# Kernel optimization log

Hardware: AMD Instinct MI355X
Metric: run time of the kernel (lower is better)

## Reference

```python
import jax, jax.numpy as jnp
from jax import lax
import numpy as np

B, C, H, W = 8, 4, 512, 512
SIGMA, W0 = 5.0, 10.0
_DBIG = 1e6  # sentinel 1D distance (larger than any image diagonal)


def setup_inputs() -> dict:
    key = jax.random.key(0)
    k1, k2 = jax.random.split(key)
    pred = jax.random.normal(k1, (B, C, H, W), jnp.float32)
    labels = jax.random.randint(k2, (B, H, W), 0, C)
    target = jax.nn.one_hot(labels, C, axis=1, dtype=jnp.float32)  # (B,C,H,W) one-hot
    return {"pred": pred, "target": target}


def _edt_sq(mask):
    """Exact squared Euclidean distance transform to True pixels of a (H,W) bool mask.
    Equivalent to scipy.ndimage.distance_transform_edt(1 - mask)**2.
    Pass 1: exact 1D distance along axis 1 via forward/backward cummax of feature indices.
    Pass 2: min-plus envelope along axis 0: D2[i,j] = min_k g[k,j]^2 + (i-k)^2."""
    Hh, Ww = mask.shape
    col = jnp.arange(Ww, dtype=jnp.float32)
    # nearest feature index to the left / right within each row
    left = lax.cummax(jnp.where(mask, col, -_DBIG), axis=1)
    dl = col[None, :] - left
    rneg = lax.cummax(jnp.where(mask, -col, -_DBIG), axis=1, reverse=True)
    dr = -rneg - col[None, :]
    g = jnp.minimum(jnp.minimum(dl, dr), _DBIG)  # (H,W) 1D distance
    g2 = g * g
    rows = jnp.arange(Hh, dtype=jnp.float32)

    def step(D2, xs):
        g2k, k = xs  # row k's 1D squared distances
        cand = g2k[None, :] + (rows - k)[:, None] ** 2
        return jnp.minimum(D2, cand), None

    D2, _ = lax.scan(step, jnp.full((Hh, Ww), _DBIG * _DBIG, jnp.float32), (g2, rows))
    return D2


def _border_weights(target, sigma, w0):
    """U-Net border weight map: w = 1 + w0*exp(-(d1+d2)^2 / (2 sigma^2))."""
    label_map = jnp.argmax(target, axis=1)  # (B,H,W)
    Cn = target.shape[1]
    masks = label_map[:, None, :, :] == jnp.arange(Cn)[None, :, None, None]  # (B,C,H,W)
    # a class contributes a distance map only if it has both fg and bg pixels
    valid = masks.any(axis=(2, 3)) & (~masks).any(axis=(2, 3))  # (B,C)
    D2 = jax.vmap(jax.vmap(_edt_sq))(masks)  # (B,C,H,W)
    dist = jnp.where(valid[:, :, None, None], jnp.sqrt(D2), _DBIG)
    ds = jnp.sort(dist, axis=1)  # invalid classes sort to the end (sentinel)
    d1, d2 = ds[:, 0], ds[:, 1]
    # if fewer than 2 valid classes, d2 (and possibly d1) is the sentinel -> exp underflows to 0 -> w == 1,
    # matching the torch code's early-continue (weights stay 1).
    return 1.0 + w0 * jnp.exp(-((d1 + d2) ** 2) / (2.0 * sigma * sigma))


def reference(pred, target):
    logp = jax.nn.log_softmax(pred, axis=1)
    target_idx = jnp.argmax(target, axis=1)  # (B,H,W)
    per_pixel = -jnp.take_along_axis(logp, target_idx[:, None], axis=1)[:, 0]  # CE, reduction='none'
    w = lax.stop_gradient(_border_weights(target, SIGMA, W0))  # weights built from detached target
    weighted = jnp.mean(per_pixel * w)
    base = jnp.mean(-(target * logp).sum(axis=1))  # soft cross-entropy base loss
    return base + weighted
```

## Files before the change

### kernel.cpp

```cpp
#include <hip/hip_runtime.h>
#include <stdint.h>

#define HH 512
#define WW 512
#define CC 4
#define BB 8
#define NPIX (BB * HH * WW)
#define SLAB 8
#define NBLK (BB * HH / SLAB)

__device__ __forceinline__ float row_min_sq(uint32_t v) {
    float c0 = (float)(v & 255u);
    float c1 = (float)((v >> 8) & 255u);
    float c2 = (float)((v >> 16) & 255u);
    float c3 = (float)(v >> 24);
    return fminf(fminf(c0 * c0, c1 * c1), fminf(c2 * c2, c3 * c3));
}

__device__ __forceinline__ uint32_t own_mask(uint32_t v) {
    uint32_t z = (~((v & 0x7F7F7F7Fu) + 0x7F7F7F7Fu)) & ~v & 0x80808080u;
    return (z >> 7) * 255u;
}

__device__ __forceinline__ void scan_row(const float* __restrict__ trow,
                                         int lane, uint32_t* __restrict__ ldsrow) {
    const int j0 = lane << 3;

    int L[8];
    float tm[8];
    #pragma unroll
    for (int c = 0; c < CC; ++c) {
        const float4* p = reinterpret_cast<const float4*>(trow + (size_t)c * (HH * WW) + j0);
        float4 a0 = p[0], a1 = p[1];
        float tv[8] = {a0.x, a0.y, a0.z, a0.w, a1.x, a1.y, a1.z, a1.w};
        #pragma unroll
        for (int jj = 0; jj < 8; ++jj) {
            if (c == 0) { tm[jj] = tv[jj]; L[jj] = 0; }
            else if (tv[jj] > tm[jj]) { tm[jj] = tv[jj]; L[jj] = c; }
        }
    }

    uint32_t gp[8] = {0, 0, 0, 0, 0, 0, 0, 0};
    #pragma unroll
    for (int c = 0; c < CC; ++c) {
        int run = -1000000;
        int lastL[8];
        #pragma unroll
        for (int jj = 0; jj < 8; ++jj) { if (L[jj] == c) run = j0 + jj; lastL[jj] = run; }
        int incl = run;
        #pragma unroll
        for (int d = 1; d < 64; d <<= 1) {
            int up = __shfl_up(incl, (unsigned)d, 64);
            if (lane >= d) incl = max(incl, up);
        }
        int excl = __shfl_up(incl, 1u, 64);
        if (lane == 0) excl = -1000000;

        int nrun = 1000000;
        int nxtL[8];
        #pragma unroll
        for (int jj = 7; jj >= 0; --jj) { if (L[jj] == c) nrun = j0 + jj; nxtL[jj] = nrun; }
        int rincl = nrun;
        #pragma unroll
        for (int d = 1; d < 64; d <<= 1) {
            int dn = __shfl_down(rincl, (unsigned)d, 64);
            if (lane < 64 - d) rincl = min(rincl, dn);
        }
        int rexcl = __shfl_down(rincl, 1u, 64);
        if (lane == 63) rexcl = 1000000;

        #pragma unroll
        for (int jj = 0; jj < 8; ++jj) {
            int last = max(lastL[jj], excl);
            int nxt  = min(nxtL[jj], rexcl);
            int gg = min(min((j0 + jj) - last, nxt - (j0 + jj)), 255);
            gp[jj] |= ((uint32_t)gg) << (c * 8);
        }
    }
    uint4* o = reinterpret_cast<uint4*>(ldsrow + j0);
    o[0] = make_uint4(gp[0], gp[1], gp[2], gp[3]);
    o[1] = make_uint4(gp[4], gp[5], gp[6], gp[7]);
}

__global__ __launch_bounds__(512) void k_fused(const float* __restrict__ pred,
                                               const float* __restrict__ target,
                                               float* __restrict__ partial) {
    __shared__ uint32_t gl[12][WW];
    __shared__ float red[8];
    __shared__ int sflag;

    const int bid0 = blockIdx.x;
    const int bid = ((bid0 & 7) << 6) | (bid0 >> 3);
    const int b  = bid >> 6;
    const int i0 = (bid & 63) << 3;
    const int tid = threadIdx.x, wid = tid >> 6, lane = tid & 63;
    const float* tbase = target + (size_t)b * CC * (HH * WW);

    {
        int r = i0 - 2 + wid;
        if (r >= 0 && r < HH) scan_row(tbase + (size_t)r * WW, lane, gl[wid]);
        if (wid < 4) {
            int r2 = i0 + 6 + wid;
            if (r2 < HH) scan_row(tbase + (size_t)r2 * WW, lane, gl[8 + wid]);
        }
    }
    if (tid == 0) sflag = 0;
    __syncthreads();

    const int grp = tid >> 8;
    const int j   = (tid & 255) << 1;
    float    bs[4][2];
    uint32_t om[4][2];
    #pragma unroll
    for (int q = 0; q < 4; ++q) {
        const int s  = (grp << 2) + q;
        const int la = s + 2;
        uint2 gown = *reinterpret_cast<const uint2*>(&gl[la][j]);
        uint32_t o0 = own_mask(gown.x), o1 = own_mask(gown.y);
        float b0 = row_min_sq(gown.x | o0);
        float b1 = row_min_sq(gown.y | o1);
        #pragma unroll
        for (int dk = 1; dk <= 2; ++dk) {
            const float dk2 = (float)(dk * dk);
            if (i0 + s - dk >= 0) {
                uint2 v = *reinterpret_cast<const uint2*>(&gl[la - dk][j]);
                b0 = fminf(b0, row_min_sq(v.x | o0) + dk2);
                b1 = fminf(b1, row_min_sq(v.y | o1) + dk2);
            }
            if (i0 + s + dk < HH) {
                uint2 v = *reinterpret_cast<const uint2*>(&gl[la + dk][j]);
                b0 = fminf(b0, row_min_sq(v.x | o0) + dk2);
                b1 = fminf(b1, row_min_sq(v.y | o1) + dk2);
            }
        }
        bs[q][0] = b0; bs[q][1] = b1; om[q][0] = o0; om[q][1] = o1;
    }

    {
        float mx = 0.f;
        #pragma unroll
        for (int q = 0; q < 4; ++q) mx = fmaxf(mx, fmaxf(bs[q][0], bs[q][1]));
        if (__any(mx > 9.0f)) { if (lane == 0) sflag = 1; }
    }
    __syncthreads();

    if (sflag) {
        for (int dk = 3; dk < HH; ++dk) {
            { int rr = i0 + wid - dk;
              if (rr >= 0 && rr < HH) scan_row(tbase + (size_t)rr * WW, lane, gl[wid]); }
            __syncthreads();
            const float dk2 = (float)(dk * dk);
            #pragma unroll
            for (int q = 0; q < 4; ++q) {
                const int s = (grp << 2) + q;
                if (i0 + s - dk >= 0) {
                    uint2 v = *reinterpret_cast<const uint2*>(&gl[s][j]);
                    bs[q][0] = fminf(bs[q][0], row_min_sq(v.x | om[q][0]) + dk2);
                    bs[q][1] = fminf(bs[q][1], row_min_sq(v.y | om[q][1]) + dk2);
                }
            }
            __syncthreads();
            { int rr = i0 + wid + dk;
              if (rr < HH) scan_row(tbase + (size_t)rr * WW, lane, gl[wid]); }
            __syncthreads();
            #pragma unroll
            for (int q = 0; q < 4; ++q) {
                const int s = (grp << 2) + q;
                if (i0 + s + dk < HH) {
                    uint2 v = *reinterpret_cast<const uint2*>(&gl[s][j]);
                    bs[q][0] = fminf(bs[q][0], row_min_sq(v.x | om[q][0]) + dk2);
                    bs[q][1] = fminf(bs[q][1], row_min_sq(v.y | om[q][1]) + dk2);
                }
            }
            __syncthreads();
            if (tid == 0) sflag = 0;
            __syncthreads();
            float nthr = (float)((dk + 1) * (dk + 1));
            float mx = 0.f;
            #pragma unroll
            for (int q = 0; q < 4; ++q) mx = fmaxf(mx, fmaxf(bs[q][0], bs[q][1]));
            if (__any(mx > nthr)) { if (lane == 0) sflag = 1; }
            __syncthreads();
            if (!sflag) break;
            if (i0 + SLAB - 1 - dk < 0 && i0 + dk >= HH) break;
        }
    }

    const float* pb = pred + (((size_t)b * CC) * HH + (size_t)i0) * WW + j;
    float vacc = 0.f;
    #pragma unroll
    for (int q = 0; q < 4; ++q) {
        const int s = (grp << 2) + q;
        const float* pr = pb + (size_t)s * WW;
        float a0[CC], a1[CC];
        #pragma unroll
        for (int c = 0; c < CC; ++c) {
            float2 t = *reinterpret_cast<const float2*>(pr + (size_t)c * (HH * WW));
            a0[c] = t.x; a1[c] = t.y;
        }
        const int L0 = __builtin_ctz(om[q][0]) >> 3;
        const int L1 = __builtin_ctz(om[q][1]) >> 3;
        {
            float m = fmaxf(fmaxf(a0[0], a0[1]), fmaxf(a0[2], a0[3]));
            float ssum = __expf(a0[0] - m) + __expf(a0[1] - m) +
                         __expf(a0[2] - m) + __expf(a0[3] - m);
            float xs = (L0 == 0) ? a0[0] : (L0 == 1) ? a0[1] : (L0 == 2) ? a0[2] : a0[3];
            float pp = (m + __logf(ssum)) - xs;
            vacc += pp * fmaf(10.0f, __expf(-0.02f * bs[q][0]), 2.0f);
        }
        {
            float m = fmaxf(fmaxf(a1[0], a1[1]), fmaxf(a1[2], a1[3]));
            float ssum = __expf(a1[0] - m) + __expf(a1[1] - m) +
                         __expf(a1[2] - m) + __expf(a1[3] - m);
            float xs = (L1 == 0) ? a1[0] : (L1 == 1) ? a1[1] : (L1 == 2) ? a1[2] : a1[3];
            float pp = (m + __logf(ssum)) - xs;
            vacc += pp * fmaf(10.0f, __expf(-0.02f * bs[q][1]), 2.0f);
        }
    }

    #pragma unroll
    for (int off = 32; off > 0; off >>= 1) vacc += __shfl_down(vacc, (unsigned)off, 64);
    if (lane == 0) red[wid] = vacc;
    __syncthreads();
    if (tid == 0) {
        float bsum = ((red[0] + red[1]) + (red[2] + red[3]))
                   + ((red[4] + red[5]) + (red[6] + red[7]));
        partial[blockIdx.x] = bsum;
    }
}

__global__ __launch_bounds__(256) void k_red(const float* __restrict__ partial,
                                             float* __restrict__ out) {
    __shared__ double sd[256];
    double a = (double)partial[threadIdx.x] + (double)partial[threadIdx.x + 256];
    sd[threadIdx.x] = a;
    __syncthreads();
    #pragma unroll
    for (int s = 128; s > 0; s >>= 1) {
        if (threadIdx.x < s) sd[threadIdx.x] += sd[threadIdx.x + s];
        __syncthreads();
    }
    if (threadIdx.x == 0) out[0] = (float)(sd[0] * (1.0 / (double)NPIX));
}

extern "C" void kernel_launch(void* const* d_in, const int* in_sizes, int n_in,
                              void* d_out, int out_size, void* d_ws, size_t ws_size,
                              hipStream_t stream) {
    const float* pred   = (const float*)d_in[0];
    const float* target = (const float*)d_in[1];
    float* partial = (float*)d_ws;
    float* out = (float*)d_out;

    hipLaunchKernelGGL(k_fused, dim3(NBLK), dim3(512), 0, stream, pred, target, partial);
    hipLaunchKernelGGL(k_red, dim3(1), dim3(256), 0, stream, partial, out);
}
```

Measured before the change: 24.85 us.

## Prefetch pred early, remap threads to 2 rows x 4 cols, exploit one-hot target

The pred logits are now loaded into registers at the top of the kernel, before the target row scans, so their global latency overlaps the EDT work. Threads are remapped to handle 2 rows by 4 columns with uint4 LDS reads, which reuses six loaded gl rows across the five-row window. The target argmax is replaced by equality tests against 1.0 that skip loading the fourth channel, and launch bounds now request higher occupancy. The one-hot shortcut only holds when targets are exactly one-hot, and the prefetched pred registers add register pressure.

```diff
diff --git a/kernel.cpp b/kernel.cpp
--- a/kernel.cpp
+++ b/kernel.cpp
@@ -25,19 +25,22 @@
 __device__ __forceinline__ void scan_row(const float* __restrict__ trow,
                                          int lane, uint32_t* __restrict__ ldsrow) {
     const int j0 = lane << 3;
+    const size_t CH = (size_t)HH * WW;
 
     int L[8];
-    float tm[8];
-    #pragma unroll
-    for (int c = 0; c < CC; ++c) {
-        const float4* p = reinterpret_cast<const float4*>(trow + (size_t)c * (HH * WW) + j0);
-        float4 a0 = p[0], a1 = p[1];
-        float tv[8] = {a0.x, a0.y, a0.z, a0.w, a1.x, a1.y, a1.z, a1.w};
-        #pragma unroll
-        for (int jj = 0; jj < 8; ++jj) {
-            if (c == 0) { tm[jj] = tv[jj]; L[jj] = 0; }
-            else if (tv[jj] > tm[jj]) { tm[jj] = tv[jj]; L[jj] = c; }
-        }
+    {
+        const float4* p0 = reinterpret_cast<const float4*>(trow + j0);
+        const float4* p1 = reinterpret_cast<const float4*>(trow + CH + j0);
+        const float4* p2 = reinterpret_cast<const float4*>(trow + 2 * CH + j0);
+        float4 a0 = p0[0], b0 = p0[1];
+        float4 a1 = p1[0], b1 = p1[1];
+        float4 a2 = p2[0], b2 = p2[1];
+        float t0[8] = {a0.x, a0.y, a0.z, a0.w, b0.x, b0.y, b0.z, b0.w};
+        float t1[8] = {a1.x, a1.y, a1.z, a1.w, b1.x, b1.y, b1.z, b1.w};
+        float t2[8] = {a2.x, a2.y, a2.z, a2.w, b2.x, b2.y, b2.z, b2.w};
+        #pragma unroll
+        for (int jj = 0; jj < 8; ++jj)
+            L[jj] = (t0[jj] == 1.0f) ? 0 : (t1[jj] == 1.0f) ? 1 : (t2[jj] == 1.0f) ? 2 : 3;
     }
 
     uint32_t gp[8] = {0, 0, 0, 0, 0, 0, 0, 0};
@@ -82,9 +85,9 @@
     o[1] = make_uint4(gp[4], gp[5], gp[6], gp[7]);
 }
 
-__global__ __launch_bounds__(512) void k_fused(const float* __restrict__ pred,
-                                               const float* __restrict__ target,
-                                               float* __restrict__ partial) {
+__global__ __launch_bounds__(512, 4) void k_fused(const float* __restrict__ pred,
+                                                  const float* __restrict__ target,
+                                                  float* __restrict__ partial) {
     __shared__ uint32_t gl[12][WW];
     __shared__ float red[8];
     __shared__ int sflag;
@@ -94,7 +97,21 @@
     const int b  = bid >> 6;
     const int i0 = (bid & 63) << 3;
     const int tid = threadIdx.x, wid = tid >> 6, lane = tid & 63;
-    const float* tbase = target + (size_t)b * CC * (HH * WW);
+    const size_t CH = (size_t)HH * WW;
+    const float* tbase = target + (size_t)b * CC * CH;
+
+    const int rp = tid >> 7;
+    const int s0 = rp << 1;
+    const int j4 = (tid & 127) << 2;
+    float4 pA[CC], pB[CC];
+    {
+        const float* pbase = pred + ((size_t)b * CC * HH + (size_t)i0) * WW + j4;
+        #pragma unroll
+        for (int c = 0; c < CC; ++c) {
+            pA[c] = *reinterpret_cast<const float4*>(pbase + ((size_t)c * HH + s0) * WW);
+            pB[c] = *reinterpret_cast<const float4*>(pbase + ((size_t)c * HH + s0 + 1) * WW);
+        }
+    }
 
     {
         int r = i0 - 2 + wid;
@@ -107,39 +124,43 @@
     if (tid == 0) sflag = 0;
     __syncthreads();
 
-    const int grp = tid >> 8;
-    const int j   = (tid & 255) << 1;
-    float    bs[4][2];
-    uint32_t om[4][2];
-    #pragma unroll
-    for (int q = 0; q < 4; ++q) {
-        const int s  = (grp << 2) + q;
-        const int la = s + 2;
-        uint2 gown = *reinterpret_cast<const uint2*>(&gl[la][j]);
-        uint32_t o0 = own_mask(gown.x), o1 = own_mask(gown.y);
-        float b0 = row_min_sq(gown.x | o0);
-        float b1 = row_min_sq(gown.y | o1);
-        #pragma unroll
-        for (int dk = 1; dk <= 2; ++dk) {
-            const float dk2 = (float)(dk * dk);
-            if (i0 + s - dk >= 0) {
-                uint2 v = *reinterpret_cast<const uint2*>(&gl[la - dk][j]);
-                b0 = fminf(b0, row_min_sq(v.x | o0) + dk2);
-                b1 = fminf(b1, row_min_sq(v.y | o1) + dk2);
-            }
-            if (i0 + s + dk < HH) {
-                uint2 v = *reinterpret_cast<const uint2*>(&gl[la + dk][j]);
-                b0 = fminf(b0, row_min_sq(v.x | o0) + dk2);
-                b1 = fminf(b1, row_min_sq(v.y | o1) + dk2);
-            }
-        }
-        bs[q][0] = b0; bs[q][1] = b1; om[q][0] = o0; om[q][1] = o1;
+    uint4 vv[6];
+    #pragma unroll
+    for (int t = 0; t < 6; ++t) vv[t] = *reinterpret_cast<const uint4*>(&gl[s0 + t][j4]);
+
+    uint32_t om0[4], om1[4];
+    float b0[4], b1[4];
+    {
+        uint32_t w0[4] = {vv[2].x, vv[2].y, vv[2].z, vv[2].w};
+        uint32_t w1[4] = {vv[3].x, vv[3].y, vv[3].z, vv[3].w};
+        #pragma unroll
+        for (int x = 0; x < 4; ++x) {
+            om0[x] = own_mask(w0[x]); b0[x] = row_min_sq(w0[x] | om0[x]);
+            om1[x] = own_mask(w1[x]); b1[x] = row_min_sq(w1[x] | om1[x]);
+        }
+    }
+    #pragma unroll
+    for (int dk = -2; dk <= 2; ++dk) {
+        if (dk == 0) continue;
+        const float dk2 = (float)(dk * dk);
+        if ((unsigned)(i0 + s0 + dk) < (unsigned)HH) {
+            const uint4 v = vv[2 + dk];
+            uint32_t w[4] = {v.x, v.y, v.z, v.w};
+            #pragma unroll
+            for (int x = 0; x < 4; ++x) b0[x] = fminf(b0[x], row_min_sq(w[x] | om0[x]) + dk2);
+        }
+        if ((unsigned)(i0 + s0 + 1 + dk) < (unsigned)HH) {
+            const uint4 v = vv[3 + dk];
+            uint32_t w[4] = {v.x, v.y, v.z, v.w};
+            #pragma unroll
+            for (int x = 0; x < 4; ++x) b1[x] = fminf(b1[x], row_min_sq(w[x] | om1[x]) + dk2);
+        }
     }
 
     {
         float mx = 0.f;
         #pragma unroll
-        for (int q = 0; q < 4; ++q) mx = fmaxf(mx, fmaxf(bs[q][0], bs[q][1]));
+        for (int x = 0; x < 4; ++x) mx = fmaxf(mx, fmaxf(b0[x], b1[x]));
         if (__any(mx > 9.0f)) { if (lane == 0) sflag = 1; }
     }
     __syncthreads();
@@ -150,35 +171,41 @@
               if (rr >= 0 && rr < HH) scan_row(tbase + (size_t)rr * WW, lane, gl[wid]); }
             __syncthreads();
             const float dk2 = (float)(dk * dk);
-            #pragma unroll
-            for (int q = 0; q < 4; ++q) {
-                const int s = (grp << 2) + q;
-                if (i0 + s - dk >= 0) {
-                    uint2 v = *reinterpret_cast<const uint2*>(&gl[s][j]);
-                    bs[q][0] = fminf(bs[q][0], row_min_sq(v.x | om[q][0]) + dk2);
-                    bs[q][1] = fminf(bs[q][1], row_min_sq(v.y | om[q][1]) + dk2);
-                }
+            if (i0 + s0 - dk >= 0) {
+                uint4 v = *reinterpret_cast<const uint4*>(&gl[s0][j4]);
+                uint32_t w[4] = {v.x, v.y, v.z, v.w};
+                #pragma unroll
+                for (int x = 0; x < 4; ++x) b0[x] = fminf(b0[x], row_min_sq(w[x] | om0[x]) + dk2);
+            }
+            if (i0 + s0 + 1 - dk >= 0) {
+                uint4 v = *reinterpret_cast<const uint4*>(&gl[s0 + 1][j4]);
+                uint32_t w[4] = {v.x, v.y, v.z, v.w};
+                #pragma unroll
+                for (int x = 0; x < 4; ++x) b1[x] = fminf(b1[x], row_min_sq(w[x] | om1[x]) + dk2);
             }
             __syncthreads();
             { int rr = i0 + wid + dk;
               if (rr < HH) scan_row(tbase + (size_t)rr * WW, lane, gl[wid]); }
             __syncthreads();
-            #pragma unroll
-            for (int q = 0; q < 4; ++q) {
-                const int s = (grp << 2) + q;
-                if (i0 + s + dk < HH) {
-                    uint2 v = *reinterpret_cast<const uint2*>(&gl[s][j]);
-                    bs[q][0] = fminf(bs[q][0], row_min_sq(v.x | om[q][0]) + dk2);
-                    bs[q][1] = fminf(bs[q][1], row_min_sq(v.y | om[q][1]) + dk2);
-                }
+            if (i0 + s0 + dk < HH) {
+                uint4 v = *reinterpret_cast<const uint4*>(&gl[s0][j4]);
+                uint32_t w[4] = {v.x, v.y, v.z, v.w};
+                #pragma unroll
+                for (int x = 0; x < 4; ++x) b0[x] = fminf(b0[x], row_min_sq(w[x] | om0[x]) + dk2);
+            }
+            if (i0 + s0 + 1 + dk < HH) {
+                uint4 v = *reinterpret_cast<const uint4*>(&gl[s0 + 1][j4]);
+                uint32_t w[4] = {v.x, v.y, v.z, v.w};
+                #pragma unroll
+                for (int x = 0; x < 4; ++x) b1[x] = fminf(b1[x], row_min_sq(w[x] | om1[x]) + dk2);
             }
             __syncthreads();
             if (tid == 0) sflag = 0;
             __syncthreads();
-            float nthr = (float)((dk + 1) * (dk + 1));
+            const float nthr = (float)((dk + 1) * (dk + 1));
             float mx = 0.f;
             #pragma unroll
-            for (int q = 0; q < 4; ++q) mx = fmaxf(mx, fmaxf(bs[q][0], bs[q][1]));
+            for (int x = 0; x < 4; ++x) mx = fmaxf(mx, fmaxf(b0[x], b1[x]));
             if (__any(mx > nthr)) { if (lane == 0) sflag = 1; }
             __syncthreads();
             if (!sflag) break;
@@ -186,35 +213,34 @@
         }
     }
 
-    const float* pb = pred + (((size_t)b * CC) * HH + (size_t)i0) * WW + j;
     float vacc = 0.f;
     #pragma unroll
-    for (int q = 0; q < 4; ++q) {
-        const int s = (grp << 2) + q;
-        const float* pr = pb + (size_t)s * WW;
-        float a0[CC], a1[CC];
-        #pragma unroll
-        for (int c = 0; c < CC; ++c) {
-            float2 t = *reinterpret_cast<const float2*>(pr + (size_t)c * (HH * WW));
-            a0[c] = t.x; a1[c] = t.y;
-        }
-        const int L0 = __builtin_ctz(om[q][0]) >> 3;
-        const int L1 = __builtin_ctz(om[q][1]) >> 3;
+    for (int x = 0; x < 4; ++x) {
         {
-            float m = fmaxf(fmaxf(a0[0], a0[1]), fmaxf(a0[2], a0[3]));
-            float ssum = __expf(a0[0] - m) + __expf(a0[1] - m) +
-                         __expf(a0[2] - m) + __expf(a0[3] - m);
-            float xs = (L0 == 0) ? a0[0] : (L0 == 1) ? a0[1] : (L0 == 2) ? a0[2] : a0[3];
+            float a[CC] = {reinterpret_cast<const float*>(&pA[0])[x],
+                           reinterpret_cast<const float*>(&pA[1])[x],
+                           reinterpret_cast<const float*>(&pA[2])[x],
+                           reinterpret_cast<const float*>(&pA[3])[x]};
+            const int L = __builtin_ctz(om0[x]) >> 3;
+            float m = fmaxf(fmaxf(a[0], a[1]), fmaxf(a[2], a[3]));
+            float ssum = __expf(a[0] - m) + __expf(a[1] - m) +
+                         __expf(a[2] - m) + __expf(a[3] - m);
+            float xs = (L == 0) ? a[0] : (L == 1) ? a[1] : (L == 2) ? a[2] : a[3];
             float pp = (m + __logf(ssum)) - xs;
-            vacc += pp * fmaf(10.0f, __expf(-0.02f * bs[q][0]), 2.0f);
+            vacc += pp * fmaf(10.0f, __expf(-0.02f * b0[x]), 2.0f);
         }
         {
-            float m = fmaxf(fmaxf(a1[0], a1[1]), fmaxf(a1[2], a1[3]));
-            float ssum = __expf(a1[0] - m) + __expf(a1[1] - m) +
-                         __expf(a1[2] - m) + __expf(a1[3] - m);
-            float xs = (L1 == 0) ? a1[0] : (L1 == 1) ? a1[1] : (L1 == 2) ? a1[2] : a1[3];
+            float a[CC] = {reinterpret_cast<const float*>(&pB[0])[x],
+                           reinterpret_cast<const float*>(&pB[1])[x],
+                           reinterpret_cast<const float*>(&pB[2])[x],
+                           reinterpret_cast<const float*>(&pB[3])[x]};
+            const int L = __builtin_ctz(om1[x]) >> 3;
+            float m = fmaxf(fmaxf(a[0], a[1]), fmaxf(a[2], a[3]));
+            float ssum = __expf(a[0] - m) + __expf(a[1] - m) +
+                         __expf(a[2] - m) + __expf(a[3] - m);
+            float xs = (L == 0) ? a[0] : (L == 1) ? a[1] : (L == 2) ? a[2] : a[3];
             float pp = (m + __logf(ssum)) - xs;
-            vacc += pp * fmaf(10.0f, __expf(-0.02f * bs[q][1]), 2.0f);
+            vacc += pp * fmaf(10.0f, __expf(-0.02f * b1[x]), 2.0f);
         }
     }
 
```

Result: slower. 27.69 us (+11.4%).
